# Optimization experiments

Measured on AMD Instinct MI355X. Metric: run time of the kernel, lower is better.

The kernel has to match this reference:

```python
import jax, jax.numpy as jnp
import numpy as np

SMALL_NUMBER = 1e-07
N, C, H, D = 100000, 128, 128, 3  # nodes, input_size, hidden_size, spatial dim


def _glorot(key, shape):
    r = np.sqrt(6.0 / (shape[-2] + shape[-1]))
    return jax.random.uniform(key, shape, dtype=jnp.float32, minval=-r, maxval=r)


def setup_inputs() -> dict:
    key = jax.random.key(0)
    ks = jax.random.split(key, 12)
    return {
        "v": jax.random.normal(ks[0], (N, C, D), dtype=jnp.float32),
        "m_v": jax.random.normal(ks[1], (N, H, D), dtype=jnp.float32),
        "Wh_z": _glorot(ks[2], (H, C)),
        "Wi_z": _glorot(ks[3], (C, C)),
        "b_z": jnp.zeros((1, C), dtype=jnp.float32),
        "Wh_r": _glorot(ks[4], (H, C)),
        "Wi_r": _glorot(ks[5], (C, C)),
        "b_r": jnp.zeros((1, C), dtype=jnp.float32),
        "Wh_v": _glorot(ks[6], (H, C)),
        "Wi_v": _glorot(ks[7], (C, C)),
        "Wq": _glorot(ks[8], (C, C)),
        "Wk": _glorot(ks[9], (C, C)),
    }


def _vlin(x, w):
    # x: [N, C_in, D], w: [C_in, C_out] -> [N, C_out, D]
    return jnp.einsum('ncd,co->nod', x, w)


def _vn_leaky(x, Wq, Wk, alpha=0.3):
    # x: [N, C, D]
    Q = jnp.einsum('ncd,cq->nqd', x, Wq)  # [N, C, D]
    K = jnp.einsum('ncd,ck->nkd', x, Wk)  # [N, C, D]
    inner = jnp.einsum('ncd,ncd->nc', Q, K)           # [N, C]
    inner = jnp.minimum(inner, 0.0)[:, :, None]        # inner * (inner < 0)
    k_norm = jnp.linalg.norm(K, axis=-1)[:, :, None] + SMALL_NUMBER  # [N, C, 1]
    out = Q - inner * K / jnp.square(k_norm)
    return alpha * x + (1.0 - alpha) * out


def reference(v, m_v, Wh_z, Wi_z, b_z, Wh_r, Wi_r, b_r, Wh_v, Wi_v, Wq, Wk):
    z = _vlin(m_v, Wh_z) + _vlin(v, Wi_z)                       # [N, C, D]
    z = jax.nn.sigmoid(jnp.linalg.norm(z, axis=-1) + b_z)[:, :, None]  # [N, C, 1]
    r = _vlin(m_v, Wh_r) + _vlin(v, Wi_r)
    r = jax.nn.sigmoid(jnp.linalg.norm(r, axis=-1) + b_r)[:, :, None]
    delta_v = _vlin(m_v, Wh_v) + _vlin(r * v, Wi_v)
    delta_v = _vn_leaky(delta_v, Wq, Wk)
    return (1.0 - z) * v + z * delta_v
```

## Files before the change

### kernel.cpp

```cpp
#include <hip/hip_runtime.h>


#define NN   100000
#define NT   16
#define NBLK (NN / NT)
#define PSZ  16384
#define FS   520
#define TSZ  (12 * FS)
#define GAP  32

typedef unsigned short us;
typedef us     us8    __attribute__((ext_vector_type(8)));
typedef __bf16 bf16x8 __attribute__((ext_vector_type(8)));
typedef float  f32x4  __attribute__((ext_vector_type(4)));

#define MFMA __builtin_amdgcn_mfma_f32_16x16x32_bf16

__device__ __forceinline__ us f2b(float f) {
    union { float f; unsigned u; } x; x.f = f;
    return (us)((x.u + 0x7FFFu + ((x.u >> 16) & 1u)) >> 16);
}
__device__ __forceinline__ float b2f(us h) {
    union { unsigned u; float f; } x; x.u = ((unsigned)h) << 16;
    return x.f;
}

__global__ void prep_weights(const float* __restrict__ Whz, const float* __restrict__ Wiz,
                             const float* __restrict__ Whr, const float* __restrict__ Wir,
                             const float* __restrict__ Whv, const float* __restrict__ Wiv,
                             us* __restrict__ ws) {
    const int mid = blockIdx.x >> 3;
    const int s = ((blockIdx.x & 7) << 8) + threadIdx.x;
    const float* W; int hp, lp;
    switch (mid) {
        case 0: W = Whz; hp = 0; lp = -1; break;
        case 1: W = Wiz; hp = 1; lp = -1; break;
        case 2: W = Whr; hp = 2; lp = 3;  break;
        case 3: W = Wir; hp = 4; lp = 5;  break;
        case 4: W = Whv; hp = 6; lp = -1; break;
        default: W = Wiv; hp = 8; lp = -1; break;
    }
    const int f = s >> 6, l = s & 63;
    const int o  = (f >> 2) * 16 + (l & 15);
    const int c0 = (f & 3) * 32 + (l >> 4) * 8;
    us8 hi, lo;
#pragma unroll
    for (int j = 0; j < 8; ++j) {
        float x = W[(c0 + j) * 128 + o];
        us h = f2b(x);
        hi[j] = h;
        lo[j] = f2b(x - b2f(h));
    }
    *(us8*)(ws + hp * PSZ + s * 8) = hi;
    if (lp >= 0) *(us8*)(ws + lp * PSZ + s * 8) = lo;
}

__global__ void prep_comp(const float* __restrict__ Whv, const float* __restrict__ Wiv,
                          const float* __restrict__ Wq,  const float* __restrict__ Wk,
                          us* __restrict__ ws) {
    __shared__ float arow[128];
    const int mat = blockIdx.x >> 7;
    const int c   = blockIdx.x & 127;
    const int o   = threadIdx.x;
    const float* A = (mat & 1) ? Wiv : Whv;
    const float* B = (mat & 2) ? Wk  : Wq;
    arow[o] = A[c * 128 + o];
    __syncthreads();
    float a0 = 0.f, a1 = 0.f, a2 = 0.f, a3 = 0.f;
#pragma unroll 8
    for (int k = 0; k < 128; k += 4) {
        a0 += arow[k + 0] * B[(k + 0) * 128 + o];
        a1 += arow[k + 1] * B[(k + 1) * 128 + o];
        a2 += arow[k + 2] * B[(k + 2) * 128 + o];
        a3 += arow[k + 3] * B[(k + 3) * 128 + o];
    }
    float t = (a0 + a1) + (a2 + a3);
    const int f = (o >> 4) * 4 + (c >> 5);
    const int l = (((c >> 3) & 3) << 4) + (o & 15);
    const int off = (f * 64 + l) * 8 + (c & 7);
    static const int hpt[4] = {10, 11, 12, 14};
    const int hp = hpt[mat];
    us h = f2b(t);
    ws[hp * PSZ + off] = h;
    if (mat & 2) ws[(hp + 1) * PSZ + off] = f2b(t - b2f(h));
}

template <int P0, int P1, int P2, int P3>
__device__ __forceinline__ void loadB4P(const us* __restrict__ ws, int wbk, bf16x8* B) {
    B[0] = *(const bf16x8*)(ws + P0 * PSZ + wbk);
    B[1] = *(const bf16x8*)(ws + P1 * PSZ + wbk);
    B[2] = *(const bf16x8*)(ws + P2 * PSZ + wbk);
    B[3] = *(const bf16x8*)(ws + P3 * PSZ + wbk);
}
__device__ __forceinline__ void p2_half(const us* __restrict__ Ah, const us* __restrict__ Al,
                                        const bf16x8* B, int kf, int ab,
                                        f32x4* dacc, f32x4* qacc, f32x4* kacc) {
#pragma unroll
    for (int m = 0; m < 3; ++m) {
        const int fo = (m * 4 + kf) * FS + ab;
        bf16x8 ah = *(const bf16x8*)(Ah + fo);
        bf16x8 al = *(const bf16x8*)(Al + fo);
        dacc[m] = MFMA(ah, B[0], dacc[m], 0, 0, 0);
        qacc[m] = MFMA(ah, B[1], qacc[m], 0, 0, 0);
        kacc[m] = MFMA(ah, B[2], kacc[m], 0, 0, 0);
        kacc[m] = MFMA(al, B[2], kacc[m], 0, 0, 0);
        kacc[m] = MFMA(ah, B[3], kacc[m], 0, 0, 0);
    }
}

__device__ __forceinline__ void loadB4(const us* __restrict__ p, int wb, bf16x8* d) {
#pragma unroll
    for (int kf = 0; kf < 4; ++kf) d[kf] = *(const bf16x8*)(p + wb + kf * 512);
}
__device__ __forceinline__ void mm_zr(const us* __restrict__ Ah, const us* __restrict__ Al,
                                      const bf16x8* bz, const bf16x8* bh, const bf16x8* bl,
                                      f32x4* zacc, f32x4* racc, int ab) {
#pragma unroll
    for (int kf = 0; kf < 4; ++kf)
#pragma unroll
        for (int m = 0; m < 3; ++m) {
            bf16x8 ah = *(const bf16x8*)(Ah + (m * 4 + kf) * FS + ab);
            bf16x8 al = *(const bf16x8*)(Al + (m * 4 + kf) * FS + ab);
            zacc[m] = MFMA(ah, bz[kf], zacc[m], 0, 0, 0);
            racc[m] = MFMA(ah, bh[kf], racc[m], 0, 0, 0);
            racc[m] = MFMA(al, bh[kf], racc[m], 0, 0, 0);
            racc[m] = MFMA(ah, bl[kf], racc[m], 0, 0, 0);
        }
}

__global__ __launch_bounds__(512, 4) void gru_vn_fused(
    const float* __restrict__ v, const float* __restrict__ mv,
    const float* __restrict__ bz, const float* __restrict__ br,
    const us* __restrict__ ws, float* __restrict__ out)
{
    __shared__ __align__(16) us pool[4 * TSZ + GAP];
    __shared__ __align__(16) float r_t[128 * 17];

    us* const vth = pool;
    us* const vtl = pool + TSZ;
    us* const mvh = pool + 2 * TSZ + GAP;
    us* const mvl = pool + 3 * TSZ + GAP;

    const int tid  = threadIdx.x;
    const int lane = tid & 63;
    const int wave = tid >> 6;
    const int arow = lane & 15;
    const int bo   = wave * 16 + arow;
    const int rsub = (lane >> 4) * 4;
    const int ab   = lane * 8;
    const int wb   = wave * 2048 + lane * 8;
    const int n0   = blockIdx.x * NT;

    const us* pWhz  = ws;            const us* pWiz  = ws + 1 * PSZ;
    const us* pWhrh = ws + 2 * PSZ;  const us* pWhrl = ws + 3 * PSZ;
    const us* pWirh = ws + 4 * PSZ;  const us* pWirl = ws + 5 * PSZ;

    {
        const int which = tid & 1;
        const int c8    = (tid >> 1) & 15;
        const int ind   = tid >> 5;
        const float* src = (which ? mv : v) + (size_t)(n0 + ind) * 384 + c8 * 24;
        float x[24];
#pragma unroll
        for (int t = 0; t < 6; ++t) *(float4*)(x + 4 * t) = *(const float4*)(src + 4 * t);
        us* const dh = which ? mvh : vth;
        us* const dl = which ? mvl : vtl;
        const int f0  = c8 >> 2;
        const int row = ind + ((c8 & 3) << 4);
#pragma unroll
        for (int d = 0; d < 3; ++d) {
            us8 hh, ll;
#pragma unroll
            for (int j = 0; j < 8; ++j) {
                float xv = x[j * 3 + d];
                __bf16 h = (__bf16)xv;
                hh[j] = __builtin_bit_cast(us, h);
                ll[j] = __builtin_bit_cast(us, (__bf16)(xv - (float)h));
            }
            const int off = (d * 4 + f0) * FS + row * 8;
            *(us8*)(dh + off) = hh;
            *(us8*)(dl + off) = ll;
        }
    }
    const float bzv = bz[bo], brv = br[bo];
    const f32x4 Z4 = {0.f, 0.f, 0.f, 0.f};

    bf16x8 Bz[4], Brh[4], Brl[4];
    loadB4(pWhz, wb, Bz); loadB4(pWhrh, wb, Brh); loadB4(pWhrl, wb, Brl);
    __syncthreads();

    f32x4 zacc[3] = {Z4, Z4, Z4}, racc[3] = {Z4, Z4, Z4};
    mm_zr(mvh, mvl, Bz, Brh, Brl, zacc, racc, ab);
    loadB4(pWiz, wb, Bz); loadB4(pWirh, wb, Brh); loadB4(pWirl, wb, Brl);
    mm_zr(vth, vtl, Bz, Brh, Brl, zacc, racc, ab);

    const int vbase = (bo >> 5) * FS + (rsub + (((bo >> 3) & 3) << 4)) * 8 + (bo & 7);
    float zz[4], vout[4][3];
#pragma unroll
    for (int q = 0; q < 4; ++q) {
        float h0 = zacc[0][q], h1 = zacc[1][q], h2 = zacc[2][q];
        zz[q] = 1.f / (1.f + __expf(-(sqrtf(h0 * h0 + h1 * h1 + h2 * h2) + bzv)));
        float r0 = racc[0][q], r1 = racc[1][q], r2 = racc[2][q];
        float rr = 1.f / (1.f + __expf(-(sqrtf(r0 * r0 + r1 * r1 + r2 * r2) + brv)));
        r_t[bo * 17 + rsub + q] = rr;
#pragma unroll
        for (int d = 0; d < 3; ++d) {
            int off = vbase + d * 4 * FS + q * 8;
            vout[q][d] = b2f(vth[off]) + b2f(vtl[off]);
        }
    }
    bf16x8 B[2][4];
    loadB4P<6, 10, 12, 13>(ws, wb, B[0]);
    __syncthreads();

#pragma unroll
    for (int it = 0; it < 2; ++it) {
        int s = tid + it * 512;
        if (s < 768) {
            int f = s >> 6, l = s & 63;
            int i = l & 15, cb = ((f & 3) << 5) + ((l >> 4) << 3);
            int off = f * FS + l * 8;
            us8 vh8 = *(const us8*)(vth + off);
            us8 vl8 = *(const us8*)(vtl + off);
            us8 oh, ol;
#pragma unroll
            for (int j = 0; j < 8; ++j) {
                float p = r_t[(cb + j) * 17 + i] * (b2f(vh8[j]) + b2f(vl8[j]));
                __bf16 h = (__bf16)p;
                oh[j] = __builtin_bit_cast(us, h);
                ol[j] = __builtin_bit_cast(us, (__bf16)(p - (float)h));
            }
            *(us8*)(vth + off) = oh;
            *(us8*)(vtl + off) = ol;
        }
    }

    f32x4 dacc[3] = {Z4, Z4, Z4}, qacc[3] = {Z4, Z4, Z4}, kacc[3] = {Z4, Z4, Z4};
#pragma unroll
    for (int kf = 0; kf < 4; ++kf) {
        const int cur = kf & 1, nxt = cur ^ 1;
        if (kf < 3) loadB4P<6, 10, 12, 13>(ws, wb + (kf + 1) * 512, B[nxt]);
        else        loadB4P<8, 11, 14, 15>(ws, wb, B[nxt]);
        p2_half(mvh, mvl, B[cur], kf, ab, dacc, qacc, kacc);
    }
    __syncthreads();

#pragma unroll
    for (int kf = 0; kf < 4; ++kf) {
        const int cur = kf & 1, nxt = cur ^ 1;
        if (kf < 3) loadB4P<8, 11, 14, 15>(ws, wb + (kf + 1) * 512, B[nxt]);
        p2_half(vth, vtl, B[cur], kf, ab, dacc, qacc, kacc);
    }

#pragma unroll
    for (int q = 0; q < 4; ++q) {
        const int i = rsub + q;
        float q0 = qacc[0][q], q1 = qacc[1][q], q2 = qacc[2][q];
        float k0 = kacc[0][q], k1 = kacc[1][q], k2 = kacc[2][q];
        float inner = fminf(q0 * k0 + q1 * k1 + q2 * k2, 0.f);
        float kn = sqrtf(k0 * k0 + k1 * k1 + k2 * k2) + 1e-7f;
        float s = inner / (kn * kn);
        float z = zz[q];
        float dv0 = 0.3f * dacc[0][q] + 0.7f * (q0 - s * k0);
        float dv1 = 0.3f * dacc[1][q] + 0.7f * (q1 - s * k1);
        float dv2 = 0.3f * dacc[2][q] + 0.7f * (q2 - s * k2);
        float* op = out + ((size_t)(n0 + i) * 128 + bo) * 3;
        op[0] = (1.f - z) * vout[q][0] + z * dv0;
        op[1] = (1.f - z) * vout[q][1] + z * dv1;
        op[2] = (1.f - z) * vout[q][2] + z * dv2;
    }
}

extern "C" void kernel_launch(void* const* d_in, const int* in_sizes, int n_in,
                              void* d_out, int out_size, void* d_ws, size_t ws_size,
                              hipStream_t stream) {
    (void)in_sizes; (void)n_in; (void)ws_size; (void)out_size;
    us* ws = (us*)d_ws;
    prep_weights<<<48, 256, 0, stream>>>(
        (const float*)d_in[2], (const float*)d_in[3],
        (const float*)d_in[5], (const float*)d_in[6],
        (const float*)d_in[8], (const float*)d_in[9], ws);
    prep_comp<<<512, 128, 0, stream>>>(
        (const float*)d_in[8],  (const float*)d_in[9],
        (const float*)d_in[10], (const float*)d_in[11], ws);
    gru_vn_fused<<<NBLK, 512, 0, stream>>>(
        (const float*)d_in[0], (const float*)d_in[1],
        (const float*)d_in[4], (const float*)d_in[7],
        ws, (float*)d_out);
}
```

Before: 242.5 us.

## Fuse m_v-side gate and delta GEMMs into one pass over shared A tiles

Merges the m_v contributions to z, r, delta, Q and K into a single k-loop, so each m_v A fragment is read from LDS once and feeds nine MFMAs instead of being reloaded in two separate phases. The v-side z/r pass and the r*v pass stay separate. This cuts LDS reads and removes one phase, but it keeps five accumulator sets live at the same time and holds seven B fragments per step, which raises register pressure under the 512-thread, 4-block launch bound. It also drops the double-buffered B prefetch, so weight load latency may be less well hidden.

```diff
diff --git a/kernel.cpp b/kernel.cpp
--- a/kernel.cpp
+++ b/kernel.cpp
@@ -85,6 +85,12 @@
     if (mat & 2) ws[(hp + 1) * PSZ + off] = f2b(t - b2f(h));
 }
 
+template <int P0, int P1, int P2>
+__device__ __forceinline__ void loadB3P(const us* __restrict__ ws, int wbk, bf16x8* B) {
+    B[0] = *(const bf16x8*)(ws + P0 * PSZ + wbk);
+    B[1] = *(const bf16x8*)(ws + P1 * PSZ + wbk);
+    B[2] = *(const bf16x8*)(ws + P2 * PSZ + wbk);
+}
 template <int P0, int P1, int P2, int P3>
 __device__ __forceinline__ void loadB4P(const us* __restrict__ ws, int wbk, bf16x8* B) {
     B[0] = *(const bf16x8*)(ws + P0 * PSZ + wbk);
@@ -92,7 +98,52 @@
     B[2] = *(const bf16x8*)(ws + P2 * PSZ + wbk);
     B[3] = *(const bf16x8*)(ws + P3 * PSZ + wbk);
 }
-__device__ __forceinline__ void p2_half(const us* __restrict__ Ah, const us* __restrict__ Al,
+template <int P0, int P1, int P2, int P3, int P4, int P5, int P6>
+__device__ __forceinline__ void loadB7P(const us* __restrict__ ws, int wbk, bf16x8* B) {
+    B[0] = *(const bf16x8*)(ws + P0 * PSZ + wbk);
+    B[1] = *(const bf16x8*)(ws + P1 * PSZ + wbk);
+    B[2] = *(const bf16x8*)(ws + P2 * PSZ + wbk);
+    B[3] = *(const bf16x8*)(ws + P3 * PSZ + wbk);
+    B[4] = *(const bf16x8*)(ws + P4 * PSZ + wbk);
+    B[5] = *(const bf16x8*)(ws + P5 * PSZ + wbk);
+    B[6] = *(const bf16x8*)(ws + P6 * PSZ + wbk);
+}
+
+__device__ __forceinline__ void mv_step(const us* __restrict__ Ah, const us* __restrict__ Al,
+                                        const bf16x8* B, int kf, int ab,
+                                        f32x4* zacc, f32x4* racc,
+                                        f32x4* dacc, f32x4* qacc, f32x4* kacc) {
+#pragma unroll
+    for (int m = 0; m < 3; ++m) {
+        const int fo = (m * 4 + kf) * FS + ab;
+        bf16x8 ah = *(const bf16x8*)(Ah + fo);
+        bf16x8 al = *(const bf16x8*)(Al + fo);
+        zacc[m] = MFMA(ah, B[0], zacc[m], 0, 0, 0);
+        racc[m] = MFMA(ah, B[1], racc[m], 0, 0, 0);
+        racc[m] = MFMA(al, B[1], racc[m], 0, 0, 0);
+        racc[m] = MFMA(ah, B[2], racc[m], 0, 0, 0);
+        dacc[m] = MFMA(ah, B[3], dacc[m], 0, 0, 0);
+        qacc[m] = MFMA(ah, B[4], qacc[m], 0, 0, 0);
+        kacc[m] = MFMA(ah, B[5], kacc[m], 0, 0, 0);
+        kacc[m] = MFMA(al, B[5], kacc[m], 0, 0, 0);
+        kacc[m] = MFMA(ah, B[6], kacc[m], 0, 0, 0);
+    }
+}
+__device__ __forceinline__ void zr_step(const us* __restrict__ Ah, const us* __restrict__ Al,
+                                        const bf16x8* B, int kf, int ab,
+                                        f32x4* zacc, f32x4* racc) {
+#pragma unroll
+    for (int m = 0; m < 3; ++m) {
+        const int fo = (m * 4 + kf) * FS + ab;
+        bf16x8 ah = *(const bf16x8*)(Ah + fo);
+        bf16x8 al = *(const bf16x8*)(Al + fo);
+        zacc[m] = MFMA(ah, B[0], zacc[m], 0, 0, 0);
+        racc[m] = MFMA(ah, B[1], racc[m], 0, 0, 0);
+        racc[m] = MFMA(al, B[1], racc[m], 0, 0, 0);
+        racc[m] = MFMA(ah, B[2], racc[m], 0, 0, 0);
+    }
+}
+__device__ __forceinline__ void rv_step(const us* __restrict__ Ah, const us* __restrict__ Al,
                                         const bf16x8* B, int kf, int ab,
                                         f32x4* dacc, f32x4* qacc, f32x4* kacc) {
 #pragma unroll
@@ -108,26 +159,6 @@
     }
 }
 
-__device__ __forceinline__ void loadB4(const us* __restrict__ p, int wb, bf16x8* d) {
-#pragma unroll
-    for (int kf = 0; kf < 4; ++kf) d[kf] = *(const bf16x8*)(p + wb + kf * 512);
-}
-__device__ __forceinline__ void mm_zr(const us* __restrict__ Ah, const us* __restrict__ Al,
-                                      const bf16x8* bz, const bf16x8* bh, const bf16x8* bl,
-                                      f32x4* zacc, f32x4* racc, int ab) {
-#pragma unroll
-    for (int kf = 0; kf < 4; ++kf)
-#pragma unroll
-        for (int m = 0; m < 3; ++m) {
-            bf16x8 ah = *(const bf16x8*)(Ah + (m * 4 + kf) * FS + ab);
-            bf16x8 al = *(const bf16x8*)(Al + (m * 4 + kf) * FS + ab);
-            zacc[m] = MFMA(ah, bz[kf], zacc[m], 0, 0, 0);
-            racc[m] = MFMA(ah, bh[kf], racc[m], 0, 0, 0);
-            racc[m] = MFMA(al, bh[kf], racc[m], 0, 0, 0);
-            racc[m] = MFMA(ah, bl[kf], racc[m], 0, 0, 0);
-        }
-}
-
 __global__ __launch_bounds__(512, 4) void gru_vn_fused(
     const float* __restrict__ v, const float* __restrict__ mv,
     const float* __restrict__ bz, const float* __restrict__ br,
@@ -150,10 +181,6 @@
     const int ab   = lane * 8;
     const int wb   = wave * 2048 + lane * 8;
     const int n0   = blockIdx.x * NT;
-
-    const us* pWhz  = ws;            const us* pWiz  = ws + 1 * PSZ;
-    const us* pWhrh = ws + 2 * PSZ;  const us* pWhrl = ws + 3 * PSZ;
-    const us* pWirh = ws + 4 * PSZ;  const us* pWirl = ws + 5 * PSZ;
 
     {
         const int which = tid & 1;
@@ -185,14 +212,25 @@
     const float bzv = bz[bo], brv = br[bo];
     const f32x4 Z4 = {0.f, 0.f, 0.f, 0.f};
 
-    bf16x8 Bz[4], Brh[4], Brl[4];
-    loadB4(pWhz, wb, Bz); loadB4(pWhrh, wb, Brh); loadB4(pWhrl, wb, Brl);
+    bf16x8 B7[7];
+    loadB7P<0, 2, 3, 6, 10, 12, 13>(ws, wb, B7);
     __syncthreads();
 
     f32x4 zacc[3] = {Z4, Z4, Z4}, racc[3] = {Z4, Z4, Z4};
-    mm_zr(mvh, mvl, Bz, Brh, Brl, zacc, racc, ab);
-    loadB4(pWiz, wb, Bz); loadB4(pWirh, wb, Brh); loadB4(pWirl, wb, Brl);
-    mm_zr(vth, vtl, Bz, Brh, Brl, zacc, racc, ab);
+    f32x4 dacc[3] = {Z4, Z4, Z4}, qacc[3] = {Z4, Z4, Z4}, kacc[3] = {Z4, Z4, Z4};
+    mv_step(mvh, mvl, B7, 0, ab, zacc, racc, dacc, qacc, kacc);
+#pragma unroll
+    for (int kf = 1; kf < 4; ++kf) {
+        loadB7P<0, 2, 3, 6, 10, 12, 13>(ws, wb + kf * 512, B7);
+        mv_step(mvh, mvl, B7, kf, ab, zacc, racc, dacc, qacc, kacc);
+    }
+
+#pragma unroll
+    for (int kf = 0; kf < 4; ++kf) {
+        bf16x8 B3[3];
+        loadB3P<1, 4, 5>(ws, wb + kf * 512, B3);
+        zr_step(vth, vtl, B3, kf, ab, zacc, racc);
+    }
 
     const int vbase = (bo >> 5) * FS + (rsub + (((bo >> 3) & 3) << 4)) * 8 + (bo & 7);
     float zz[4], vout[4][3];
@@ -209,8 +247,8 @@
             vout[q][d] = b2f(vth[off]) + b2f(vtl[off]);
         }
     }
-    bf16x8 B[2][4];
-    loadB4P<6, 10, 12, 13>(ws, wb, B[0]);
+    bf16x8 B4[4];
+    loadB4P<8, 11, 14, 15>(ws, wb, B4);
     __syncthreads();
 
 #pragma unroll
@@ -234,22 +272,13 @@
             *(us8*)(vtl + off) = ol;
         }
     }
-
-    f32x4 dacc[3] = {Z4, Z4, Z4}, qacc[3] = {Z4, Z4, Z4}, kacc[3] = {Z4, Z4, Z4};
-#pragma unroll
-    for (int kf = 0; kf < 4; ++kf) {
-        const int cur = kf & 1, nxt = cur ^ 1;
-        if (kf < 3) loadB4P<6, 10, 12, 13>(ws, wb + (kf + 1) * 512, B[nxt]);
-        else        loadB4P<8, 11, 14, 15>(ws, wb, B[nxt]);
-        p2_half(mvh, mvl, B[cur], kf, ab, dacc, qacc, kacc);
-    }
     __syncthreads();
 
-#pragma unroll
-    for (int kf = 0; kf < 4; ++kf) {
-        const int cur = kf & 1, nxt = cur ^ 1;
-        if (kf < 3) loadB4P<8, 11, 14, 15>(ws, wb + (kf + 1) * 512, B[nxt]);
-        p2_half(vth, vtl, B[cur], kf, ab, dacc, qacc, kacc);
+    rv_step(vth, vtl, B4, 0, ab, dacc, qacc, kacc);
+#pragma unroll
+    for (int kf = 1; kf < 4; ++kf) {
+        loadB4P<8, 11, 14, 15>(ws, wb + kf * 512, B4);
+        rv_step(vth, vtl, B4, kf, ab, dacc, qacc, kacc);
     }
 
 #pragma unroll
```

Result: no change. 238.0 us (-1.9%).
